# Optimization experiments

Hardware: AMD Instinct MI355X
Metric: run time of the kernel (lower is better)

## Reference

```python
import jax, jax.numpy as jnp
import numpy as np

B = 8192          # batch
CIN = 256         # in_channels
COUT = 64         # out_channels
K = 3             # kernel_size
NK = 4            # num_kernels
HIDDEN = int(CIN * 0.25)   # attention hidden = int(in_channels*ratio) = 64
TEMP = 34.0       # attention temperature
KAN_IN = 64 * 4   # base*4 = flattened conv output (COUT*2*2)
GRID_SIZE, SPLINE_ORDER = 5, 3
GMIN, GMAX = -1.0, 1.0
NUM_BASES = GRID_SIZE + SPLINE_ORDER  # 8


def setup_inputs() -> dict:
    key = jax.random.key(0)
    ks = jax.random.split(key, 8)
    s = 0.05
    return {
        "x": jax.random.normal(ks[0], (B, CIN, 4, 4), jnp.float32),
        # dynamic-conv kernel bank [num_kernels, out, in, k, k]
        "weight": jax.random.normal(ks[1], (NK, COUT, CIN, K, K), jnp.float32) * s,
        "bias": jnp.zeros((NK, COUT), jnp.float32),
        # Attention2D: GAP -> fc1 (1x1 conv == linear) -> ReLU -> fc2 -> softmax(/T)
        "fc1_w": jax.random.normal(ks[2], (HIDDEN, CIN), jnp.float32) * s,
        "fc1_b": jnp.zeros((HIDDEN,), jnp.float32),
        "fc2_w": jax.random.normal(ks[3], (NK, HIDDEN), jnp.float32) * s,
        "fc2_b": jnp.zeros((NK,), jnp.float32),
        # KANLinear params (efficient-KAN style)
        "kan_base_w": jax.random.normal(ks[4], (COUT, KAN_IN), jnp.float32) * s,
        "kan_spline_w": jax.random.normal(ks[5], (COUT, KAN_IN, NUM_BASES), jnp.float32) * s,
        "kan_spline_scaler": jnp.ones((COUT, KAN_IN), jnp.float32),
    }


def _bspline_bases(x):
    """Cox-de Boor B-spline bases; x [B, F] -> [B, F, GRID_SIZE+SPLINE_ORDER]."""
    h = (GMAX - GMIN) / GRID_SIZE
    # extended grid, shared across features: length grid_size + 2*order + 1 = 12
    grid = jnp.arange(-SPLINE_ORDER, GRID_SIZE + SPLINE_ORDER + 1, dtype=x.dtype) * h + GMIN
    xe = x[..., None]  # [B, F, 1]
    bases = ((xe >= grid[:-1]) & (xe < grid[1:])).astype(x.dtype)  # order 0
    for k in range(1, SPLINE_ORDER + 1):
        left = (xe - grid[: -(k + 1)]) / (grid[k:-1] - grid[: -(k + 1)]) * bases[..., :-1]
        right = (grid[k + 1:] - xe) / (grid[k + 1:] - grid[1:-k]) * bases[..., 1:]
        bases = left + right
    return bases  # [B, F, 8]


def reference(x, weight, bias, fc1_w, fc1_b, fc2_w, fc2_b,
              kan_base_w, kan_spline_w, kan_spline_scaler):
    b = x.shape[0]
    # --- Attention2D: softmax over kernel bank ---
    pooled = x.mean(axis=(2, 3))                                  # [B, CIN]
    hid = jax.nn.relu(pooled @ fc1_w.T + fc1_b)                   # [B, HIDDEN]
    attn = jax.nn.softmax((hid @ fc2_w.T + fc2_b) / TEMP, axis=-1)  # [B, NK]
    # --- per-sample dynamic conv, fused form ---
    # sum_k a[b,k] * conv(x, W_k) == conv with per-sample aggregated weight
    w_all = weight.reshape(NK * COUT, CIN, K, K)
    y = jax.lax.conv_general_dilated(
        x, w_all, window_strides=(1, 1), padding="VALID",
        dimension_numbers=("NCHW", "OIHW", "NCHW"))                # [B, NK*COUT, 2, 2]
    y = y.reshape(b, NK, COUT, y.shape[-2], y.shape[-1])
    conv_out = jnp.einsum("bk,bkohw->bohw", attn, y)
    conv_out = conv_out + (attn @ bias)[:, :, None, None]          # aggregated bias
    # --- KANLinear on flattened conv output ---
    feat = conv_out.reshape(b, -1)                                 # [B, 256]
    base_out = jax.nn.silu(feat) @ kan_base_w.T                    # [B, COUT]
    bases = _bspline_bases(feat)                                   # [B, 256, 8]
    spline_out = jnp.einsum("big,oig->bo", bases,
                            kan_spline_w * kan_spline_scaler[..., None])
    return base_out + spline_out                                   # [B, COUT]
```

## Files before the change

kernel.cpp:

```cpp
#include <hip/hip_runtime.h>

#define BT   8192
#define MS   8
#define XBUF (MS * 656)

typedef _Float16 half8  __attribute__((ext_vector_type(8)));
typedef _Float16 half4v __attribute__((ext_vector_type(4)));
typedef float    floatx4  __attribute__((ext_vector_type(4)));
typedef float    floatx16 __attribute__((ext_vector_type(16)));

__global__ __launch_bounds__(256) void prep_kernel(
    const float* __restrict__ weight, const float* __restrict__ base_w,
    const float* __restrict__ spline_w, const float* __restrict__ scaler,
    const float* __restrict__ fc1_w,
    _Float16* __restrict__ W3, _Float16* __restrict__ Wk3,
    _Float16* __restrict__ Wf3)
{
    const int bb = blockIdx.x;
    const int tid = threadIdx.x;
    if (bb < 256) {
        const int n = bb;
        const int c = tid;
        const float* src = weight + ((size_t)n * 256 + c) * 9;
        const int cc = c >> 5, ci = c & 31;
        #pragma unroll
        for (int ij = 0; ij < 9; ++ij) {
            W3[((size_t)(cc * 9 + ij) * 256 + n) * 32 + ci] = (_Float16)src[ij];
        }
    } else if (bb < 328) {
        const int st = bb - 256;
        #pragma unroll
        for (int u = 0; u < 8; ++u) {
            const int idx = u * 256 + tid;
            const int n = idx >> 5, kk = idx & 31;
            const int k = st * 32 + kk;
            float v;
            if (k < 256) {
                v = base_w[n * 256 + k];
            } else {
                const int r = k - 256;
                const int i = r >> 3, g = r & 7;
                v = spline_w[((size_t)n * 256 + i) * 8 + g] * scaler[n * 256 + i];
            }
            Wk3[(size_t)st * 2048 + idx] = (_Float16)v;
        }
    } else {
        const int st2 = bb - 328;
        #pragma unroll
        for (int u = 0; u < 8; ++u) {
            const int idx = u * 256 + tid;
            const int n = idx >> 5, kk = idx & 31;
            Wf3[(size_t)st2 * 2048 + idx] = (_Float16)fc1_w[n * 256 + st2 * 32 + kk];
        }
    }
}

__device__ __forceinline__ void bases8c(float xv, _Float16* dst) {
    const float t = (xv + 2.2f) * 2.5f;
    const float ft = floorf(t);
    const int idx = (int)ft;
    const float u = t - ft, v = 1.f - u;
    const float u2 = u * u, v2 = v * v;
    const float c3 = u2 * u * (1.f / 6.f);
    const float c2 = (1.f / 6.f) + 0.5f * (u + u2 - u2 * u);
    const float c1 = (1.f / 6.f) + 0.5f * (v + v2 - v2 * v);
    const float c0 = v2 * v * (1.f / 6.f);
    half8 hb;
    #pragma unroll
    for (int tt = 0; tt < 8; ++tt) {
        const int d = idx - tt;
        float b = 0.f;
        b = (d == 0) ? c3 : b;
        b = (d == 1) ? c2 : b;
        b = (d == 2) ? c1 : b;
        b = (d == 3) ? c0 : b;
        hb[tt] = (_Float16)b;
    }
    *(half8*)dst = hb;
}

__global__ __launch_bounds__(256, 4) void fused_kernel(
    const float* __restrict__ x, const _Float16* __restrict__ W3,
    const _Float16* __restrict__ Wk3, const _Float16* __restrict__ Wf3,
    const float* __restrict__ bias, const float* __restrict__ fc1_b,
    const float* __restrict__ fc2_w, const float* __restrict__ fc2_b,
    float* __restrict__ out)
{
    __shared__ __align__(16) char smem[MS * 2312 * 2];
    __shared__ float hid_lds[MS * 68];
    __shared__ float attn_s[MS][4];

    _Float16* Xs  = (_Float16*)smem;
    _Float16* Pl  = (_Float16*)(smem + 2 * XBUF * 2);
    _Float16* Act = (_Float16*)smem;

    const int tid = threadIdx.x;
    const int wv = tid >> 6, lane = tid & 63;
    const int nl = lane & 15, q = lane >> 4;
    const int b0i = blockIdx.x * MS;

    const int posr = nl & 3;
    const int aLane = (nl >> 2) * 656 + ((posr >> 1) * 4 + (posr & 1)) * 40 + q * 8;
    const int lbW = ((wv * 4) * 16 + nl) * 32 + q * 8;

    const int s_ = tid >> 5, cch = tid & 31;
    const float* xg = x + ((size_t)(b0i + s_) * 256 + cch) * 16;

    floatx4 acc[2][4];
    #pragma unroll
    for (int rt = 0; rt < 2; ++rt)
        #pragma unroll
        for (int t = 0; t < 4; ++t)
            acc[rt][t] = floatx4{0.f, 0.f, 0.f, 0.f};

    half8 b0[4], b1[4];
    #pragma unroll
    for (int t = 0; t < 4; ++t)
        b0[t] = *(const half8*)(W3 + lbW + t * 512);
    #pragma unroll
    for (int t = 0; t < 4; ++t)
        b1[t] = *(const half8*)(W3 + 8192 + lbW + t * 512);

    floatx16 r = *(const floatx16*)xg;
    {
        _Float16* xd = &Xs[s_ * 656 + cch];
        #pragma unroll
        for (int p = 0; p < 16; ++p) xd[p * 40] = (_Float16)r[p];
        float sm = 0.f;
        #pragma unroll
        for (int p = 0; p < 16; ++p) sm += r[p];
        Pl[s_ * 264 + cch] = (_Float16)(sm * (1.0f / 16.0f));
    }
    r = *(const floatx16*)(xg + 512);
    __syncthreads();

    #pragma unroll 1
    for (int cc = 0; cc < 8; ++cc) {
        const int cur = cc & 1;
        if (cc < 7) {
            _Float16* xd = &Xs[(cur ^ 1) * XBUF + s_ * 656 + cch];
            #pragma unroll
            for (int p = 0; p < 16; ++p) xd[p * 40] = (_Float16)r[p];
            float sm = 0.f;
            #pragma unroll
            for (int p = 0; p < 16; ++p) sm += r[p];
            Pl[s_ * 264 + (cc + 1) * 32 + cch] = (_Float16)(sm * (1.0f / 16.0f));
        }
        if (cc < 6) r = *(const floatx16*)(xg + (cc + 2) * 512);

        const _Float16* wst = W3 + (size_t)cc * 9 * 8192 + lbW;
        const _Float16* xb = &Xs[cur * XBUF + aLane];

        const int p0tab[9] = {0, 1, 2, 4, 5, 6, 8, 9, 10};

        #pragma unroll
        for (int ij = 0; ij < 9; ++ij) {
            const _Float16* wnx = (cc * 9 + ij + 2 < 72)
                                ? (wst + (size_t)(ij + 2) * 8192)
                                : (W3 + lbW);
            half8 b2[4];
            #pragma unroll
            for (int t = 0; t < 4; ++t)
                b2[t] = *(const half8*)(wnx + t * 512);

            const int p0 = p0tab[ij];
            const half8 aF0 = *(const half8*)&xb[p0 * 40];
            const half8 aF1 = *(const half8*)&xb[2624 + p0 * 40];
            #pragma unroll
            for (int t = 0; t < 4; ++t)
                acc[0][t] = __builtin_amdgcn_mfma_f32_16x16x32_f16(aF0, b0[t], acc[0][t], 0, 0, 0);
            #pragma unroll
            for (int t = 0; t < 4; ++t)
                acc[1][t] = __builtin_amdgcn_mfma_f32_16x16x32_f16(aF1, b0[t], acc[1][t], 0, 0, 0);
            #pragma unroll
            for (int t = 0; t < 4; ++t) { b0[t] = b1[t]; b1[t] = b2[t]; }
        }
        __syncthreads();
    }

    {
        floatx4 a1 = floatx4{0.f, 0.f, 0.f, 0.f};
        const _Float16* wfb = Wf3 + ((wv * 16 + nl) * 32 + q * 8);
        const _Float16* pb = &Pl[(nl & 7) * 264 + q * 8];
        #pragma unroll
        for (int st = 0; st < 8; ++st) {
            const half8 aF = *(const half8*)(pb + st * 32);
            const half8 bF = *(const half8*)(wfb + st * 2048);
            a1 = __builtin_amdgcn_mfma_f32_16x16x32_f16(aF, bF, a1, 0, 0, 0);
        }
        if (q < 2) {
            const int h = wv * 16 + nl;
            const float fb = fc1_b[h];
            #pragma unroll
            for (int reg = 0; reg < 4; ++reg)
                hid_lds[(q * 4 + reg) * 68 + h] = fmaxf(a1[reg] + fb, 0.f);
        }
    }
    __syncthreads();

    if (wv == 0 && lane < 32) {
        const int s = lane >> 2, kb = lane & 3;
        float l = fc2_b[kb];
        #pragma unroll 8
        for (int h = 0; h < 64; ++h) l += hid_lds[s * 68 + h] * fc2_w[kb * 64 + h];
        float m = fmaxf(l, __shfl_xor(l, 1));
        m = fmaxf(m, __shfl_xor(m, 2));
        const float e = __expf((l - m) * (1.0f / 34.0f));
        float sm = e + __shfl_xor(e, 1);
        sm += __shfl_xor(sm, 2);
        attn_s[s][kb] = e / sm;
    }
    #pragma unroll
    for (int rt = 0; rt < 2; ++rt) {
        const int s = rt * 4 + q;
        #pragma unroll
        for (int t = 0; t < 4; ++t) {
            #pragma unroll
            for (int e = 0; e < 4; ++e) {
                const int f = (t * 16 + nl) * 4 + e;
                float* fp = (float*)&Act[s * 2312 + 256 + f * 8];
                fp[wv] = acc[rt][t][e];
            }
        }
    }
    __syncthreads();

    {
        const int sl = lane >> 5, fl = lane & 31;
        const int s = wv * 2 + sl;
        const float a0 = attn_s[s][0], a1 = attn_s[s][1],
                    a2 = attn_s[s][2], a3 = attn_s[s][3];
        const int o0 = fl * 2, f0 = fl * 8;
        const float badd0 = a0 * bias[o0] + a1 * bias[64 + o0]
                          + a2 * bias[128 + o0] + a3 * bias[192 + o0];
        const float badd1 = a0 * bias[o0 + 1] + a1 * bias[64 + o0 + 1]
                          + a2 * bias[128 + o0 + 1] + a3 * bias[192 + o0 + 1];
        half8 sv;
        #pragma unroll
        for (int u = 0; u < 8; ++u) {
            float* fp = (float*)&Act[s * 2312 + 256 + (f0 + u) * 8];
            const floatx4 P = *(const floatx4*)fp;
            const float fv = a0 * P[0] + a1 * P[1] + a2 * P[2] + a3 * P[3]
                           + ((u < 4) ? badd0 : badd1);
            const float ex = __expf(-fv);
            sv[u] = (_Float16)(fv * __builtin_amdgcn_rcpf(1.f + ex));
            bases8c(fv, (_Float16*)fp);
        }
        *(half8*)&Act[s * 2312 + o0 * 4] = sv;
    }
    __syncthreads();

    {
        floatx4 a2 = floatx4{0.f, 0.f, 0.f, 0.f};
        const _Float16* wkb = Wk3 + ((size_t)(wv * 16 + nl) * 32 + q * 8);
        const _Float16* ab = &Act[(nl & 7) * 2312 + q * 8];
        half8 kb0 = *(const half8*)(wkb);
        half8 kb1 = *(const half8*)(wkb + 2048);
        #pragma unroll 4
        for (int i = 0; i < 72; ++i) {
            half8 kb2;
            if (i < 70) kb2 = *(const half8*)(wkb + (size_t)(i + 2) * 2048);
            const half8 aF = *(const half8*)(ab + i * 32);
            a2 = __builtin_amdgcn_mfma_f32_16x16x32_f16(aF, kb0, a2, 0, 0, 0);
            kb0 = kb1; kb1 = kb2;
        }
        if (q < 2) {
            #pragma unroll
            for (int reg = 0; reg < 4; ++reg)
                out[(size_t)(b0i + q * 4 + reg) * 64 + wv * 16 + nl] = a2[reg];
        }
    }
}

extern "C" void kernel_launch(void* const* d_in, const int* in_sizes, int n_in,
                              void* d_out, int out_size, void* d_ws, size_t ws_size,
                              hipStream_t stream) {
    const float* x          = (const float*)d_in[0];
    const float* weight     = (const float*)d_in[1];
    const float* bias       = (const float*)d_in[2];
    const float* fc1_w      = (const float*)d_in[3];
    const float* fc1_b      = (const float*)d_in[4];
    const float* fc2_w      = (const float*)d_in[5];
    const float* fc2_b      = (const float*)d_in[6];
    const float* kan_base_w = (const float*)d_in[7];
    const float* kan_spline = (const float*)d_in[8];
    const float* kan_scaler = (const float*)d_in[9];
    float* out = (float*)d_out;

    _Float16* W3  = (_Float16*)d_ws;
    _Float16* Wk3 = W3 + (size_t)72 * 8192;
    _Float16* Wf3 = Wk3 + (size_t)72 * 2048;

    prep_kernel<<<336, 256, 0, stream>>>(weight, kan_base_w, kan_spline,
                                         kan_scaler, fc1_w, W3, Wk3, Wf3);
    fused_kernel<<<BT / MS, 256, 0, stream>>>(x, W3, Wk3, Wf3, bias, fc1_b,
                                              fc2_w, fc2_b, out);
}
```

Measured before the change: 284.7 us.

## Stage full input tile in LDS upfront and deepen weight register prefetch

```diff
diff --git a/kernel.cpp b/kernel.cpp
--- a/kernel.cpp
+++ b/kernel.cpp
@@ -1,8 +1,9 @@
 #include <hip/hip_runtime.h>
 
-#define BT   8192
-#define MS   8
-#define XBUF (MS * 656)
+#define BT    8192
+#define MS    8
+#define P_STR 264
+#define S_STR 4232
 
 typedef _Float16 half8  __attribute__((ext_vector_type(8)));
 typedef _Float16 half4v __attribute__((ext_vector_type(4)));
@@ -79,19 +80,19 @@
     *(half8*)dst = hb;
 }
 
-__global__ __launch_bounds__(256, 4) void fused_kernel(
+__global__ __launch_bounds__(256, 2) void fused_kernel(
     const float* __restrict__ x, const _Float16* __restrict__ W3,
     const _Float16* __restrict__ Wk3, const _Float16* __restrict__ Wf3,
     const float* __restrict__ bias, const float* __restrict__ fc1_b,
     const float* __restrict__ fc2_w, const float* __restrict__ fc2_b,
     float* __restrict__ out)
 {
-    __shared__ __align__(16) char smem[MS * 2312 * 2];
+    __shared__ __align__(16) char smem[71936];
     __shared__ float hid_lds[MS * 68];
     __shared__ float attn_s[MS][4];
 
     _Float16* Xs  = (_Float16*)smem;
-    _Float16* Pl  = (_Float16*)(smem + 2 * XBUF * 2);
+    _Float16* Pl  = (_Float16*)(smem + 67712);
     _Float16* Act = (_Float16*)smem;
 
     const int tid = threadIdx.x;
@@ -99,12 +100,35 @@
     const int nl = lane & 15, q = lane >> 4;
     const int b0i = blockIdx.x * MS;
 
+    const int s_ = tid >> 5, c4 = tid & 31;
+    #pragma unroll
+    for (int pass = 0; pass < 2; ++pass) {
+        const int cbase = pass * 128 + c4 * 4;
+        const float* xg = x + ((size_t)(b0i + s_) * 256 + cbase) * 16;
+        const floatx16 r0 = *(const floatx16*)(xg);
+        const floatx16 r1 = *(const floatx16*)(xg + 16);
+        const floatx16 r2 = *(const floatx16*)(xg + 32);
+        const floatx16 r3 = *(const floatx16*)(xg + 48);
+        _Float16* xd = &Xs[s_ * S_STR + cbase];
+        float s0 = 0.f, s1 = 0.f, s2 = 0.f, s3 = 0.f;
+        #pragma unroll
+        for (int p = 0; p < 16; ++p) {
+            half4v w;
+            w[0] = (_Float16)r0[p]; w[1] = (_Float16)r1[p];
+            w[2] = (_Float16)r2[p]; w[3] = (_Float16)r3[p];
+            *(half4v*)&xd[p * P_STR] = w;
+            s0 += r0[p]; s1 += r1[p]; s2 += r2[p]; s3 += r3[p];
+        }
+        half4v pw;
+        pw[0] = (_Float16)(s0 * 0.0625f); pw[1] = (_Float16)(s1 * 0.0625f);
+        pw[2] = (_Float16)(s2 * 0.0625f); pw[3] = (_Float16)(s3 * 0.0625f);
+        *(half4v*)&Pl[s_ * P_STR + cbase] = pw;
+    }
+
     const int posr = nl & 3;
-    const int aLane = (nl >> 2) * 656 + ((posr >> 1) * 4 + (posr & 1)) * 40 + q * 8;
+    const int pixb = (posr >> 1) * 4 + (posr & 1);
+    const int aLane = (nl >> 2) * S_STR + pixb * P_STR + q * 8;
     const int lbW = ((wv * 4) * 16 + nl) * 32 + q * 8;
-
-    const int s_ = tid >> 5, cch = tid & 31;
-    const float* xg = x + ((size_t)(b0i + s_) * 256 + cch) * 16;
 
     floatx4 acc[2][4];
     #pragma unroll
@@ -113,59 +137,36 @@
         for (int t = 0; t < 4; ++t)
             acc[rt][t] = floatx4{0.f, 0.f, 0.f, 0.f};
 
-    half8 b0[4], b1[4];
-    #pragma unroll
-    for (int t = 0; t < 4; ++t)
-        b0[t] = *(const half8*)(W3 + lbW + t * 512);
-    #pragma unroll
-    for (int t = 0; t < 4; ++t)
-        b1[t] = *(const half8*)(W3 + 8192 + lbW + t * 512);
-
-    floatx16 r = *(const floatx16*)xg;
-    {
-        _Float16* xd = &Xs[s_ * 656 + cch];
-        #pragma unroll
-        for (int p = 0; p < 16; ++p) xd[p * 40] = (_Float16)r[p];
-        float sm = 0.f;
-        #pragma unroll
-        for (int p = 0; p < 16; ++p) sm += r[p];
-        Pl[s_ * 264 + cch] = (_Float16)(sm * (1.0f / 16.0f));
-    }
-    r = *(const floatx16*)(xg + 512);
-    __syncthreads();
-
+    const _Float16* wl = W3 + lbW;
+    half8 b0[4], b1[4], b2[4];
+    #pragma unroll
+    for (int t = 0; t < 4; ++t) b0[t] = *(const half8*)(wl + t * 512);
+    #pragma unroll
+    for (int t = 0; t < 4; ++t) b1[t] = *(const half8*)(wl + 8192 + t * 512);
+    #pragma unroll
+    for (int t = 0; t < 4; ++t) b2[t] = *(const half8*)(wl + 16384 + t * 512);
+
+    __syncthreads();
+
+    const _Float16* xbs = Xs + aLane;
     #pragma unroll 1
     for (int cc = 0; cc < 8; ++cc) {
-        const int cur = cc & 1;
-        if (cc < 7) {
-            _Float16* xd = &Xs[(cur ^ 1) * XBUF + s_ * 656 + cch];
-            #pragma unroll
-            for (int p = 0; p < 16; ++p) xd[p * 40] = (_Float16)r[p];
-            float sm = 0.f;
-            #pragma unroll
-            for (int p = 0; p < 16; ++p) sm += r[p];
-            Pl[s_ * 264 + (cc + 1) * 32 + cch] = (_Float16)(sm * (1.0f / 16.0f));
-        }
-        if (cc < 6) r = *(const floatx16*)(xg + (cc + 2) * 512);
-
-        const _Float16* wst = W3 + (size_t)cc * 9 * 8192 + lbW;
-        const _Float16* xb = &Xs[cur * XBUF + aLane];
-
+        const _Float16* xb = xbs + cc * 32;
+        const _Float16* wst = wl + (size_t)cc * 9 * 8192;
         const int p0tab[9] = {0, 1, 2, 4, 5, 6, 8, 9, 10};
-
         #pragma unroll
         for (int ij = 0; ij < 9; ++ij) {
-            const _Float16* wnx = (cc * 9 + ij + 2 < 72)
-                                ? (wst + (size_t)(ij + 2) * 8192)
-                                : (W3 + lbW);
-            half8 b2[4];
+            const _Float16* wnx = (cc * 9 + ij + 3 < 72)
+                                ? (wst + (size_t)(ij + 3) * 8192)
+                                : wl;
+            half8 b3[4];
             #pragma unroll
             for (int t = 0; t < 4; ++t)
-                b2[t] = *(const half8*)(wnx + t * 512);
-
-            const int p0 = p0tab[ij];
-            const half8 aF0 = *(const half8*)&xb[p0 * 40];
-            const half8 aF1 = *(const half8*)&xb[2624 + p0 * 40];
+                b3[t] = *(const half8*)(wnx + t * 512);
+
+            const int po = p0tab[ij] * P_STR;
+            const half8 aF0 = *(const half8*)&xb[po];
+            const half8 aF1 = *(const half8*)&xb[po + 4 * S_STR];
             #pragma unroll
             for (int t = 0; t < 4; ++t)
                 acc[0][t] = __builtin_amdgcn_mfma_f32_16x16x32_f16(aF0, b0[t], acc[0][t], 0, 0, 0);
@@ -173,15 +174,15 @@
             for (int t = 0; t < 4; ++t)
                 acc[1][t] = __builtin_amdgcn_mfma_f32_16x16x32_f16(aF1, b0[t], acc[1][t], 0, 0, 0);
             #pragma unroll
-            for (int t = 0; t < 4; ++t) { b0[t] = b1[t]; b1[t] = b2[t]; }
-        }
-        __syncthreads();
-    }
+            for (int t = 0; t < 4; ++t) { b0[t] = b1[t]; b1[t] = b2[t]; b2[t] = b3[t]; }
+        }
+    }
+    __syncthreads();
 
     {
         floatx4 a1 = floatx4{0.f, 0.f, 0.f, 0.f};
         const _Float16* wfb = Wf3 + ((wv * 16 + nl) * 32 + q * 8);
-        const _Float16* pb = &Pl[(nl & 7) * 264 + q * 8];
+        const _Float16* pb = &Pl[(nl & 7) * P_STR + q * 8];
         #pragma unroll
         for (int st = 0; st < 8; ++st) {
             const half8 aF = *(const half8*)(pb + st * 32);
```

Result: slower. 309.9 us (+8.9%).
